# Kernel tuning notes

Measured on AMD Instinct MI355X. Metric: run time of the kernel, lower is better.

## Reference

```python
import jax, jax.numpy as jnp
import numpy as np

D_MODEL = 256
GAMMA = 0.9          # ret_D is built in the torch forward but never applied to the output; kept for fidelity notes
SCALE_BASE = 512     # XPOS default
TEMP = 10000.0
TWO_PI = 2.0 * np.pi


def sine_pos_embed(x):
    """DETR-style 1D sine position embedding with an all-ones mask (as in forward).
    x: [B,T,C] -> pos: [1,T,C] (mask is [1,T] ones, so batch dim broadcasts)."""
    T, C = x.shape[1], x.shape[2]
    x_embed = jnp.arange(1, T + 1, dtype=jnp.float32)          # cumsum of ones
    x_embed = x_embed / (x_embed[-1] + 1e-6) * TWO_PI          # normalize=True
    dim_t = TEMP ** (2.0 * (jnp.arange(C) // 2).astype(jnp.float32) / C)
    pos = x_embed[:, None] / dim_t                             # [T,C]
    pos = jnp.stack([jnp.sin(pos[:, 0::2]), jnp.cos(pos[:, 1::2])], axis=2).reshape(T, C)
    return pos[None].astype(x.dtype)


def _dup_interleave(m):
    # [L, d/2] -> [L, d], columns repeated pairwise: [a,b] -> [a,a,b,b]
    return jnp.repeat(m, 2, axis=-1)


def _rotate_every_two(x):
    x1, x2 = x[..., 0::2], x[..., 1::2]
    return jnp.stack([-x2, x1], axis=-1).reshape(x.shape)


def xpos_apply(x, downscale=False):
    """RetNet XPOS rotary embedding. x: [B,L,d]."""
    L, d = x.shape[1], x.shape[2]
    half = d // 2
    scale_vec = (jnp.arange(0, d, 2, dtype=jnp.float32) + 0.4 * d) / (1.4 * d)   # [d/2]
    power = jnp.arange(L, dtype=jnp.float32) / SCALE_BASE
    scale = scale_vec[None, :] ** power[:, None]                                  # [L, d/2]
    inv_freq = 1.0 / (TEMP ** (jnp.arange(half, dtype=jnp.float32) / half))
    sinusoid = jnp.arange(L, dtype=jnp.float32)[:, None] * inv_freq[None, :]      # [L, d/2]
    sin, cos = jnp.sin(sinusoid), jnp.cos(sinusoid)
    if downscale:
        scale = 1.0 / scale
    sin_s = _dup_interleave(sin * scale)[None].astype(x.dtype)   # [1,L,d]
    cos_s = _dup_interleave(cos * scale)[None].astype(x.dtype)
    return x * cos_s + _rotate_every_two(x) * sin_s


def setup_inputs() -> dict:
    key = jax.random.key(0)
    ks = jax.random.split(key, 8)
    B, TXT, VID, D = 16, 32, 2048, D_MODEL
    S = TXT + VID
    inp = {
        "src": jax.random.normal(ks[0], (B, S, D), dtype=jnp.float32),
        "learn_vid_ret": jax.random.normal(ks[1], (VID * VID, 1), dtype=jnp.float32),
        "W_txt_Q": jax.random.normal(ks[2], (D, D), dtype=jnp.float32) / D,
        "W_txt_K": jax.random.normal(ks[3], (D, D), dtype=jnp.float32) / D,
        "W_txt_V": jax.random.normal(ks[4], (D, D), dtype=jnp.float32) / D,
        "W_vid_Q": jax.random.normal(ks[5], (D, D), dtype=jnp.float32) / D,
        "W_vid_K": jax.random.normal(ks[6], (D, D), dtype=jnp.float32) / D,
        "W_vid_V": jax.random.normal(ks[7], (D, D), dtype=jnp.float32) / D,
        "txt_length": TXT,
    }
    return inp


def reference(src, learn_vid_ret, W_txt_Q, W_txt_K, W_txt_V, W_vid_Q, W_vid_K, W_vid_V, txt_length):
    S = src.shape[1]
    vid_length = S - txt_length

    # learned retention mask over the video block
    learn_ret = jax.nn.sigmoid(learn_vid_ret.reshape(vid_length, vid_length))
    diag = jnp.eye(vid_length, dtype=src.dtype)
    video_ret = (1.0 - diag) * learn_ret
    loss_sparsity = jnp.mean(jnp.abs(video_ret))

    # full [S,S] mask: ones everywhere, sigmoid(learned) on the vid-vid block
    ret_mask = jnp.ones((S, S), dtype=src.dtype).at[txt_length:, txt_length:].set(learn_ret)

    txt_mem = src[:, :txt_length]   # [B,TXT,D]
    vid_mem = src[:, txt_length:]   # [B,VID,D]

    pos = sine_pos_embed(txt_mem)   # [1,TXT,D]
    txt_Q = (pos + txt_mem) @ W_txt_Q
    txt_K = (pos + txt_mem) @ W_txt_K
    vid_Q = xpos_apply(vid_mem @ W_vid_Q)
    vid_K = xpos_apply(vid_mem @ W_vid_K, downscale=True)

    Q = jnp.concatenate([txt_Q, vid_Q], axis=1)                  # [B,S,D]
    K = jnp.concatenate([txt_K, vid_K], axis=1)                  # [B,S,D]
    V = jnp.concatenate([txt_mem @ W_txt_V, vid_mem @ W_vid_V], axis=1)

    # retention: QK^T elementwise-masked (no softmax), then weighted V sum
    scores = jnp.einsum('bsd,btd->bst', Q, K) * ret_mask[None]   # [B,S,S]
    out = scores @ V                                             # [B,S,D]
    return out, loss_sparsity
```

## Files before the change

kernel.cpp:

```cpp
#include <hip/hip_runtime.h>

#define B_   16
#define TXT  32
#define VID  2048
#define D_   256
#define S_   2080
#define SP   2176
#define NKT  34
#define GTOT 17424

typedef unsigned short ushort_t;
typedef __attribute__((ext_vector_type(8))) short short8;
typedef __attribute__((ext_vector_type(4))) short short4v;
typedef __attribute__((ext_vector_type(4))) float f32x4;
typedef __attribute__((ext_vector_type(16))) float f32x16;

__device__ __forceinline__ ushort_t f2bf(float f) {
  unsigned u = __builtin_bit_cast(unsigned, f);
  unsigned r = (u + 0x7FFFu + ((u >> 16) & 1u)) >> 16;
  return (ushort_t)r;
}
__device__ __forceinline__ float bf2f(ushort_t h) {
  unsigned u = ((unsigned)h) << 16;
  return __builtin_bit_cast(float, u);
}

__device__ __forceinline__ void g2l16(void* lds, const void* g) {
  __builtin_amdgcn_global_load_lds(
      (const __attribute__((address_space(1))) char*)g,
      (__attribute__((address_space(3))) char*)lds, 16, 0, 0);
}

__device__ __forceinline__ f32x4 mfma16(short8 a, short8 b, f32x4 c) {
  return __builtin_amdgcn_mfma_f32_16x16x32_bf16(a, b, c, 0, 0, 0);
}
__device__ __forceinline__ f32x16 mfma32(short8 a, short8 b, f32x16 c) {
  return __builtin_amdgcn_mfma_f32_32x32x16_bf16(a, b, c, 0, 0, 0);
}


__global__ void tbl_kernel(float* __restrict__ tbl) {
  int idx = blockIdx.x * 256 + threadIdx.x;
  int n = idx >> 7, i = idx & 127;
  float invf = powf(10000.0f, -(float)i / 128.0f);
  float ang = (float)n * invf;
  float s, co;
  sincosf(ang, &s, &co);
  float sv = ((float)(2 * i) + 102.4f) / 358.4f;
  float sc = powf(sv, (float)n / 512.0f);
  float4 r;
  r.x = co * sc; r.y = s * sc; r.z = co / sc; r.w = s / sc;
  *(float4*)(tbl + (size_t)idx * 4) = r;
}

__global__ void sig_loss_kernel(const float* __restrict__ learn, ushort_t* __restrict__ sigp,
                                float* __restrict__ loss) {
  const int tid = threadIdx.x;
  const int base = (blockIdx.x * 256 + tid) * 8;
  float4 v0 = *(const float4*)(learn + base);
  float4 v1 = *(const float4*)(learn + base + 4);
  float vals[8] = {v0.x, v0.y, v0.z, v0.w, v1.x, v1.y, v1.z, v1.w};
  float acc = 0.f;
  short8 sh;
  #pragma unroll
  for (int j = 0; j < 8; ++j) {
    int idx = base + j;
    float s = 1.0f / (1.0f + expf(-vals[j]));
    sh[j] = (short)f2bf(s);
    int rr = idx >> 11, cc = idx & 2047;
    if (rr != cc) acc += s;
  }
  *(short8*)(sigp + base) = sh;
  __shared__ float red[256];
  red[tid] = acc;
  __syncthreads();
  #pragma unroll
  for (int st = 128; st > 0; st >>= 1) {
    if (tid < st) red[tid] += red[tid + st];
    __syncthreads();
  }
  if (tid == 0) atomicAdd(loss, red[0] * (1.0f / 4194304.0f));
}

__global__ void pad0_kernel(ushort_t* __restrict__ Qp, ushort_t* __restrict__ Ks,
                            ushort_t* __restrict__ VTs) {
  int i = blockIdx.x * 256 + threadIdx.x;
  short8 z = {0, 0, 0, 0, 0, 0, 0, 0};
  if (i < 49152) {
    int bb = i / 3072, rem = i - bb * 3072;
    int row = 2080 + (rem >> 5), c8 = (rem & 31) * 8;
    *(short8*)(Qp + ((size_t)bb * SP + row) * D_ + c8) = z;
  } else if (i < 65536) {
    int j = i - 49152; int bb = j >> 10; int rem = j & 1023;
    int kstep = rem >> 6, ch = rem & 63;
    size_t base = ((size_t)(bb * NKT + 32)) << 14;
    *(short8*)(Ks + base + kstep * 1024 + 512 + ch * 8) = z;
  } else if (i < 81920) {
    int j = i - 65536; int bb = j >> 10; int rem = j & 1023;
    size_t base = (((size_t)(bb * NKT + 32)) << 14) + 8192;
    *(short8*)(VTs + base + rem * 8) = z;
  }
}

__global__ void wt_kernel(const float* __restrict__ Wq, const float* __restrict__ Wk,
                          const float* __restrict__ Wv, ushort_t* __restrict__ WT) {
  __shared__ float t[64][68];
  const int k0 = blockIdx.x * 64, n0 = blockIdx.y * 64, mt = blockIdx.z;
  const float* W = (mt == 0) ? Wq : (mt == 1) ? Wk : Wv;
  int tid = threadIdx.x;
  int r = tid >> 4, cq = (tid & 15) * 4;
  #pragma unroll
  for (int m = 0; m < 4; ++m) {
    int k = m * 16 + r;
    float4 v = *(const float4*)(W + (size_t)(k0 + k) * 256 + n0 + cq);
    t[k][cq] = v.x; t[k][cq + 1] = v.y; t[k][cq + 2] = v.z; t[k][cq + 3] = v.w;
  }
  __syncthreads();
  #pragma unroll
  for (int m = 0; m < 4; ++m) {
    int n = m * 16 + r;
    short4v h;
    h[0] = (short)f2bf(t[cq + 0][n]);
    h[1] = (short)f2bf(t[cq + 1][n]);
    h[2] = (short)f2bf(t[cq + 2][n]);
    h[3] = (short)f2bf(t[cq + 3][n]);
    *(short4v*)(WT + ((size_t)mt * D_ + n0 + n) * D_ + k0 + cq) = h;
  }
}

__global__ void txt_kernel(const float* __restrict__ src,
                           const float* __restrict__ Wq, const float* __restrict__ Wk,
                           const float* __restrict__ Wv,
                           ushort_t* __restrict__ Qp, ushort_t* __restrict__ Ks,
                           ushort_t* __restrict__ VTs) {
  __shared__ float a_s[8][256];
  __shared__ float x_s[8][256];
  const int tg = blockIdx.x;
  const int b  = blockIdx.y;
  const int c  = threadIdx.x;
  #pragma unroll
  for (int t = 0; t < 8; ++t) {
    int row = tg * 8 + t;
    float x = src[((size_t)b * S_ + row) * D_ + c];
    float xe = (float)(row + 1) * (6.283185307179586f / (32.0f + 1e-6f));
    int i = c >> 1;
    float dimt = powf(10000.0f, (2.0f * (float)i) / 256.0f);
    float ang = xe / dimt;
    float pv = (c & 1) ? cosf(ang) : sinf(ang);
    x_s[t][c] = x;
    a_s[t][c] = x + pv;
  }
  __syncthreads();
  float q[8] = {0,0,0,0,0,0,0,0}, k[8] = {0,0,0,0,0,0,0,0}, v[8] = {0,0,0,0,0,0,0,0};
  for (int kk = 0; kk < 256; ++kk) {
    float wq = Wq[(size_t)kk * 256 + c];
    float wk = Wk[(size_t)kk * 256 + c];
    float wv = Wv[(size_t)kk * 256 + c];
    #pragma unroll
    for (int t = 0; t < 8; ++t) {
      q[t] = fmaf(a_s[t][kk], wq, q[t]);
      k[t] = fmaf(a_s[t][kk], wk, k[t]);
      v[t] = fmaf(x_s[t][kk], wv, v[t]);
    }
  }
  #pragma unroll
  for (int t = 0; t < 8; ++t) {
    int row = tg * 8 + t;
    Qp[((size_t)b * SP + row) * D_ + c] = f2bf(q[t]);
    size_t kidx = ((((size_t)(b * NKT)) << 14) + (c >> 4) * 1024 + row * 16 + (c & 15)) ^ (((row >> 2) & 1) << 3);
    Ks[kidx] = f2bf(k[t]);
    size_t vidx = ((((size_t)(b * NKT)) << 14) + (row >> 4) * 4096 + c * 16 + (row & 15)) ^ (((c >> 2) & 1) << 3);
    VTs[vidx] = f2bf(v[t]);
  }
}

__global__ __launch_bounds__(256, 2) void vid_gemm(
    const float* __restrict__ src, const ushort_t* __restrict__ WT,
    const float* __restrict__ tbl,
    ushort_t* __restrict__ Qp, ushort_t* __restrict__ Ks, ushort_t* __restrict__ VTs) {
  __shared__ __align__(16) ushort_t ldsA[64 * 64];
  __shared__ __align__(16) ushort_t ldsB[64 * 64];

  const int rt = blockIdx.x;
  const int b  = blockIdx.y;
  const int ct = blockIdx.z;
  const int nt = ct >> 2;
  const int n0 = (ct & 3) * 64;
  const int tid = threadIdx.x;
  const int wv = tid >> 6, lane = tid & 63, l15 = lane & 15, l4 = lane >> 4;

  f32x4 acc[4];
  #pragma unroll
  for (int t2 = 0; t2 < 4; ++t2) { acc[t2][0] = 0.f; acc[t2][1] = 0.f; acc[t2][2] = 0.f; acc[t2][3] = 0.f; }

  for (int kk = 0; kk < 256; kk += 64) {
    #pragma unroll
    for (int m = 0; m < 4; ++m) {
      int q = m * 256 + tid;
      int r = q >> 4;
      int kc = (q & 15) * 4;
      const float4 v = *(const float4*)(src + ((size_t)b * S_ + TXT + rt * 64 + r) * D_ + kk + kc);
      short4v h;
      h[0] = (short)f2bf(v.x); h[1] = (short)f2bf(v.y);
      h[2] = (short)f2bf(v.z); h[3] = (short)f2bf(v.w);
      int off = ((r << 7) + (kc << 1)) ^ ((r & 7) << 4);
      *(short4v*)((char*)ldsA + off) = h;
    }
    #pragma unroll
    for (int m = 0; m < 2; ++m) {
      int p = (m * 256 + tid) * 16;
      int nl = p >> 7;
      int c = (p & 127) ^ ((nl & 7) << 4);
      g2l16((char*)ldsB + p, (const char*)(WT + ((size_t)nt * D_ + n0 + nl) * D_ + kk) + c);
    }
    __syncthreads();
    #pragma unroll
    for (int ks = 0; ks < 2; ++ks) {
      int ar = wv * 16 + l15;
      int aoff = ((ar << 7) + ((ks * 32 + l4 * 8) << 1)) ^ ((ar & 7) << 4);
      short8 av = *(const short8*)((const char*)ldsA + aoff);
      #pragma unroll
      for (int t2 = 0; t2 < 4; ++t2) {
        int nl = t2 * 16 + l15;
        int boff = ((nl << 7) + ((ks * 32 + l4 * 8) << 1)) ^ ((nl & 7) << 4);
        short8 bv = *(const short8*)((const char*)ldsB + boff);
        acc[t2] = mfma16(av, bv, acc[t2]);
      }
    }
    __syncthreads();
  }

  const int rowl = wv * 16 + l4 * 4;
  if (nt < 2) {
    #pragma unroll
    for (int t2 = 0; t2 < 4; ++t2) {
      int c = n0 + t2 * 16 + l15;
      #pragma unroll
      for (int r = 0; r < 4; ++r) {
        int n = rt * 64 + rowl + r;
        float x = acc[t2][r];
        float xp = __shfl_xor(x, 1);
        const float4 tb = *(const float4*)(tbl + ((size_t)n * 128 + (c >> 1)) * 4);
        float cs = (nt == 0) ? tb.x : tb.z;
        float ss = (nt == 0) ? tb.y : tb.w;
        float val = (c & 1) ? fmaf(x, cs, xp * ss) : fmaf(x, cs, -xp * ss);
        if (nt == 0) {
          Qp[((size_t)b * SP + TXT + n) * D_ + c] = f2bf(val);
        } else {
          int kvg = TXT + n;
          size_t kidx = ((((size_t)(b * NKT + (kvg >> 6))) << 14) + (c >> 4) * 1024 + (kvg & 63) * 16 + (c & 15))
                        ^ (((kvg >> 2) & 1) << 3);
          Ks[kidx] = f2bf(val);
        }
      }
    }
  } else {
    #pragma unroll
    for (int t2 = 0; t2 < 4; ++t2)
      #pragma unroll
      for (int r = 0; r < 4; ++r) {
        int rr = rowl + r;
        int cc = t2 * 16 + l15;
        int off = ((rr << 7) + (cc << 1)) ^ ((rr & 7) << 4);
        *(ushort_t*)((char*)ldsA + off) = f2bf(acc[t2][r]);
      }
    __syncthreads();
    int n = tid >> 2;
    int rc = (tid & 3) * 16;
    short8 o0, o1;
    #pragma unroll
    for (int j = 0; j < 8; ++j) {
      int rr = rc + j;
      int off = ((rr << 7) + (n << 1)) ^ ((rr & 7) << 4);
      o0[j] = *(const short*)((const char*)ldsA + off);
    }
    #pragma unroll
    for (int j = 0; j < 8; ++j) {
      int rr = rc + 8 + j;
      int off = ((rr << 7) + (n << 1)) ^ ((rr & 7) << 4);
      o1[j] = *(const short*)((const char*)ldsA + off);
    }
    int d = n0 + n;
    int kvg0 = TXT + rt * 64 + rc;
    size_t base = (((size_t)(b * NKT + (kvg0 >> 6))) << 14) + ((kvg0 >> 4) & 3) * 4096 + d * 16;
    int swz8 = ((d >> 2) & 1) << 3;
    *(short8*)(VTs + base + swz8) = o0;
    *(short8*)(VTs + base + (swz8 ^ 8)) = o1;
  }
}

__global__ __launch_bounds__(512, 1) void attn_kernel(
    const ushort_t* __restrict__ Qp, const ushort_t* __restrict__ Ks,
    const ushort_t* __restrict__ VTs, const ushort_t* __restrict__ sigp,
    float* __restrict__ out) {
  __shared__ __align__(16) ushort_t Kb[2][16384];
  __shared__ __align__(16) ushort_t Vb[2][16384];
  __shared__ __align__(16) ushort_t Pb[2][4096];

  const int kblk = blockIdx.x;
  const int bs = (kblk & 7) * 32 + (kblk >> 3);
  const int gs = bs * 68 + (bs < 16 ? bs : 16);
  const int ge = gs + 68 + (bs < 16 ? 1 : 0);

  const int tid = threadIdx.x;
  const int wid = tid >> 6, lane = tid & 63;
  const int l31 = lane & 31, l5 = lane >> 5;
  const bool isQK = wid < 4;
  const int qh = (wid >> 1) & 1, kh = wid & 1;
  const int d0 = (wid & 3) * 64;

  int cb_b = gs / 1089;
  int rrem = gs - cb_b * 1089;
  int cb_q = rrem / 33;
  int cb_k = rrem - cb_q * 33;

  auto stage = [&](ushort_t* dst, const ushort_t* srcb, int bb, int tt) {
    const char* src = (const char*)srcb + (((size_t)(bb * NKT + tt)) << 15);
    #pragma unroll
    for (int m = 0; m < 4; ++m) { int s = m * 512 + tid; g2l16((char*)dst + s * 16, src + s * 16); }
  };

  short8 qf[16];
  int4 mq[4];
  const int qloc = qh * 32 + l31;

  auto ldq = [&](int bb, int qq) {
    const ushort_t* qrow = Qp + ((size_t)bb * SP + qq * 64 + qloc) * D_ + l5 * 8;
    #pragma unroll
    for (int ks = 0; ks < 16; ++ks) qf[ks] = *(const short8*)(qrow + ks * 16);
  };
  auto ldmask = [&](int qq, int tt) {
    int q = qq * 64 + qloc;
    int qc = q - TXT; qc = qc < 0 ? 0 : (qc > 2047 ? 2047 : qc);
    int kvp = tt * 64 + kh * 32 - TXT;
    int kvc = (kvp >= 0 && kvp <= 2016) ? kvp : 0;
    const int4* mrow = (const int4*)(sigp + (size_t)qc * 2048 + kvc);
    mq[0] = mrow[0]; mq[1] = mrow[1]; mq[2] = mrow[2]; mq[3] = mrow[3];
  };

  f32x16 oacc[2][2];
  #pragma unroll
  for (int i2 = 0; i2 < 2; ++i2)
    #pragma unroll
    for (int j2 = 0; j2 < 2; ++j2)
      #pragma unroll
      for (int r = 0; r < 16; ++r) oacc[i2][j2][r] = 0.f;

  const int kswz = ((l31 >> 2) & 1) << 4;
  const int pswz = (l31 & 7) << 4;

  int n1_b = cb_b, n1_q = cb_q, n1_k = cb_k;
  if (gs <= ge - 2) { ++n1_k; if (n1_k == 33) { n1_k = 0; ++n1_q; if (n1_q == 33) { n1_q = 0; ++n1_b; } } }
  stage(Kb[gs & 1], Ks, cb_b, cb_k);
  if (isQK) ldmask(cb_q, cb_k);
  stage(Kb[(gs + 1) & 1], Ks, n1_b, n1_k);
  stage(Vb[gs & 1], VTs, cb_b, cb_k);
  if (isQK) { asm volatile("s_waitcnt vmcnt(12)" ::: "memory"); }
  else      { asm volatile("s_waitcnt vmcnt(8)"  ::: "memory"); }
  __builtin_amdgcn_sched_barrier(0);
  __builtin_amdgcn_s_barrier();
  __builtin_amdgcn_sched_barrier(0);

  int pv_b = cb_b, pv_q = cb_q, pv_k = cb_k;

  for (int i = gs; i <= ge; ++i) {
    const int cb = i & 1;
    n1_b = cb_b; n1_q = cb_q; n1_k = cb_k;
    if (i <= ge - 2) { ++n1_k; if (n1_k == 33) { n1_k = 0; ++n1_q; if (n1_q == 33) { n1_q = 0; ++n1_b; } } }
    int n2_b = n1_b, n2_q = n1_q, n2_k = n1_k;
    if (i <= ge - 3) { ++n2_k; if (n2_k == 33) { n2_k = 0; ++n2_q; if (n2_q == 33) { n2_q = 0; ++n2_b; } } }

    if (isQK) {
      if (i < ge) {
        if (cb_k == 0 || i == gs) ldq(cb_b, cb_q);
        f32x16 s0, s1;
        #pragma unroll
        for (int r = 0; r < 16; ++r) { s0[r] = 0.f; s1[r] = 0.f; }
        const int krow = (kh * 32 + l31) * 32 + l5 * 16;
        __builtin_amdgcn_s_setprio(1);
        #pragma unroll
        for (int ks = 0; ks < 8; ++ks) {
          short8 ka = *(const short8*)((const char*)Kb[cb] + ((ks * 2048 + krow) ^ kswz));
          short8 kc = *(const short8*)((const char*)Kb[cb] + (((ks + 8) * 2048 + krow) ^ kswz));
          s0 = mfma32(ka, qf[ks], s0);
          s1 = mfma32(kc, qf[ks + 8], s1);
        }
        __builtin_amdgcn_s_setprio(0);
        {
          int q = cb_q * 64 + qloc;
          bool qv = (q >= TXT) && (q < S_);
          int kvp = cb_k * 64 + kh * 32 - TXT;
          bool kvv = (kvp >= 0 && kvp <= 2016);
          bool ok = qv && kvv;
          const unsigned* mw = (const unsigned*)mq;
          #pragma unroll
          for (int t = 0; t < 4; ++t) {
            unsigned w0p, w1p;
            {
              unsigned wa = mw[4 * t + 0], wb = mw[4 * t + 2];
              unsigned w = l5 ? wb : wa;
              float m0 = ok ? bf2f((ushort_t)(w & 0xFFFFu)) : 1.0f;
              float m1 = ok ? bf2f((ushort_t)(w >> 16)) : 1.0f;
              int r = 4 * t;
              float p0 = (s0[r] + s1[r]) * m0;
              float p1 = (s0[r + 1] + s1[r + 1]) * m1;
              asm("v_cvt_pk_bf16_f32 %0, %1, %2" : "=v"(w0p) : "v"(p0), "v"(p1));
            }
            {
              unsigned wa = mw[4 * t + 1], wb = mw[4 * t + 3];
              unsigned w = l5 ? wb : wa;
              float m0 = ok ? bf2f((ushort_t)(w & 0xFFFFu)) : 1.0f;
              float m1 = ok ? bf2f((ushort_t)(w >> 16)) : 1.0f;
              int r = 4 * t + 2;
              float p0 = (s0[r] + s1[r]) * m0;
              float p1 = (s0[r + 1] + s1[r + 1]) * m1;
              asm("v_cvt_pk_bf16_f32 %0, %1, %2" : "=v"(w1p) : "v"(p0), "v"(p1));
            }
            int off = ((qloc << 7) + (kh << 6) + (t << 4) + (l5 << 3)) ^ pswz;
            *(uint2*)((char*)Pb[cb] + off) = make_uint2(w0p, w1p);
          }
        }
        asm volatile("s_waitcnt lgkmcnt(0)" ::: "memory");
        __builtin_amdgcn_sched_barrier(0);
      }
    } else {
      if (i > gs) {
        const int pbuf = cb ^ 1;
        __builtin_amdgcn_s_setprio(1);
        #pragma unroll
        for (int ks = 0; ks < 4; ++ks) {
          short8 pf0 = *(const short8*)((const char*)Pb[pbuf] + ((l31 * 128 + ks * 32 + l5 * 16) ^ pswz));
          short8 pf1 = *(const short8*)((const char*)Pb[pbuf] + (((32 + l31) * 128 + ks * 32 + l5 * 16) ^ pswz));
          short8 vf0 = *(const short8*)((const char*)Vb[pbuf] + ((ks * 8192 + (d0 + l31) * 32 + l5 * 16) ^ kswz));
          short8 vf1 = *(const short8*)((const char*)Vb[pbuf] + ((ks * 8192 + (d0 + 32 + l31) * 32 + l5 * 16) ^ kswz));
          oacc[0][0] = mfma32(pf0, vf0, oacc[0][0]);
          oacc[0][1] = mfma32(pf0, vf1, oacc[0][1]);
          oacc[1][0] = mfma32(pf1, vf0, oacc[1][0]);
          oacc[1][1] = mfma32(pf1, vf1, oacc[1][1]);
        }
        __builtin_amdgcn_s_setprio(0);
        if (pv_k == 32 || i == ge) {
          #pragma unroll
          for (int qg2 = 0; qg2 < 2; ++qg2)
            #pragma unroll
            for (int dg = 0; dg < 2; ++dg)
              #pragma unroll
              for (int r = 0; r < 16; ++r) {
                int qg = pv_q * 64 + qg2 * 32 + (r & 3) + 8 * (r >> 2) + 4 * l5;
                int dd = d0 + dg * 32 + l31;
                if (qg < S_)
                  unsafeAtomicAdd(&out[((size_t)pv_b * S_ + qg) * D_ + dd], oacc[qg2][dg][r]);
                oacc[qg2][dg][r] = 0.f;
              }
        }
      }
    }

    __builtin_amdgcn_sched_barrier(0);
    __builtin_amdgcn_s_barrier();
    __builtin_amdgcn_sched_barrier(0);

    if (i < ge) {
      if (isQK) ldmask(n1_q, n1_k);
      stage(Kb[cb], Ks, n2_b, n2_k);
      stage(Vb[cb ^ 1], VTs, n1_b, n1_k);
      __builtin_amdgcn_sched_barrier(0);
      if (isQK) { asm volatile("s_waitcnt vmcnt(12)" ::: "memory"); }
      else      { asm volatile("s_waitcnt vmcnt(8)"  ::: "memory"); }
      __builtin_amdgcn_sched_barrier(0);
    }
    __builtin_amdgcn_s_barrier();
    __builtin_amdgcn_sched_barrier(0);

    pv_b = cb_b; pv_q = cb_q; pv_k = cb_k;
    cb_b = n1_b; cb_q = n1_q; cb_k = n1_k;
  }
}

extern "C" void kernel_launch(void* const* d_in, const int* in_sizes, int n_in,
                              void* d_out, int out_size, void* d_ws, size_t ws_size,
                              hipStream_t stream) {
  (void)in_sizes; (void)n_in; (void)ws_size;
  const float* src   = (const float*)d_in[0];
  const float* learn = (const float*)d_in[1];
  const float* Wtq = (const float*)d_in[2];
  const float* Wtk = (const float*)d_in[3];
  const float* Wtv = (const float*)d_in[4];
  const float* Wvq = (const float*)d_in[5];
  const float* Wvk = (const float*)d_in[6];
  const float* Wvv = (const float*)d_in[7];
  float* out = (float*)d_out;

  char* ws = (char*)d_ws;
  const size_t QKV_ONE = (size_t)B_ * SP * D_ * 2;
  const size_t QP_OFF  = 0;
  const size_t KS_OFF  = QP_OFF + QKV_ONE;
  const size_t VT_OFF  = KS_OFF + QKV_ONE;
  const size_t SIG_OFF = VT_OFF + QKV_ONE;
  const size_t TBL_OFF = SIG_OFF + (size_t)VID * VID * 2;
  const size_t WT_OFF  = TBL_OFF + (size_t)VID * 128 * 4 * sizeof(float);

  ushort_t* Qp   = (ushort_t*)(ws + QP_OFF);
  ushort_t* Ks   = (ushort_t*)(ws + KS_OFF);
  ushort_t* VTs  = (ushort_t*)(ws + VT_OFF);
  ushort_t* sigp = (ushort_t*)(ws + SIG_OFF);
  float*    tbl  = (float*)(ws + TBL_OFF);
  ushort_t* WT   = (ushort_t*)(ws + WT_OFF);

  hipMemsetAsync(d_out, 0, (size_t)out_size * sizeof(float), stream);
  pad0_kernel<<<320, 256, 0, stream>>>(Qp, Ks, VTs);
  tbl_kernel<<<1024, 256, 0, stream>>>(tbl);
  sig_loss_kernel<<<2048, 256, 0, stream>>>(learn, sigp, out + (size_t)B_ * S_ * D_);
  wt_kernel<<<dim3(4, 4, 3), 256, 0, stream>>>(Wvq, Wvk, Wvv, WT);
  txt_kernel<<<dim3(4, B_), 256, 0, stream>>>(src, Wtq, Wtk, Wtv, Qp, Ks, VTs);
  vid_gemm<<<dim3(32, B_, 12), 256, 0, stream>>>(src, WT, tbl, Qp, Ks, VTs);
  attn_kernel<<<dim3(256), 512, 0, stream>>>(Qp, Ks, VTs, sigp, out);
}
```

Baseline: 325.6 us.

## Single-buffer attention LDS for higher occupancy and pre-convert video src to bf16

The attention kernel drops double-buffered K/V shared tiles for single buffers, raises the launch-bounds occupancy hint and doubles the grid to 512 blocks, each handling half the tile range. This trades software prefetch depth for more resident blocks to hide latency. Separately, a new cvt_kernel converts the video part of src to bf16 once, so vid_gemm can stream A tiles with direct global-to-LDS copies instead of converting fp32 in each of the 12 column-tile blocks. That costs an extra kernel launch and extra workspace, and it falls back to the old path if the workspace is too small.

```diff
diff --git a/kernel.cpp b/kernel.cpp
--- a/kernel.cpp
+++ b/kernel.cpp
@@ -80,6 +80,20 @@
     __syncthreads();
   }
   if (tid == 0) atomicAdd(loss, red[0] * (1.0f / 4194304.0f));
+}
+
+__global__ void cvt_kernel(const float* __restrict__ src, ushort_t* __restrict__ srcb) {
+  int i = blockIdx.x * 256 + threadIdx.x;
+  int b = i >> 16;
+  int rem = i & 65535;
+  int row = rem >> 5, c8 = (rem & 31) * 8;
+  const float* p = src + ((size_t)b * S_ + TXT + row) * D_ + c8;
+  float4 v0 = *(const float4*)p;
+  float4 v1 = *(const float4*)(p + 4);
+  short8 h;
+  h[0] = (short)f2bf(v0.x); h[1] = (short)f2bf(v0.y); h[2] = (short)f2bf(v0.z); h[3] = (short)f2bf(v0.w);
+  h[4] = (short)f2bf(v1.x); h[5] = (short)f2bf(v1.y); h[6] = (short)f2bf(v1.z); h[7] = (short)f2bf(v1.w);
+  *(short8*)(srcb + ((size_t)b * VID + row) * D_ + c8) = h;
 }
 
 __global__ void pad0_kernel(ushort_t* __restrict__ Qp, ushort_t* __restrict__ Ks,
@@ -174,9 +188,10 @@
   }
 }
 
+template <int MODE>
 __global__ __launch_bounds__(256, 2) void vid_gemm(
-    const float* __restrict__ src, const ushort_t* __restrict__ WT,
-    const float* __restrict__ tbl,
+    const float* __restrict__ src, const ushort_t* __restrict__ srcb,
+    const ushort_t* __restrict__ WT, const float* __restrict__ tbl,
     ushort_t* __restrict__ Qp, ushort_t* __restrict__ Ks, ushort_t* __restrict__ VTs) {
   __shared__ __align__(16) ushort_t ldsA[64 * 64];
   __shared__ __align__(16) ushort_t ldsB[64 * 64];
@@ -194,17 +209,28 @@
   for (int t2 = 0; t2 < 4; ++t2) { acc[t2][0] = 0.f; acc[t2][1] = 0.f; acc[t2][2] = 0.f; acc[t2][3] = 0.f; }
 
   for (int kk = 0; kk < 256; kk += 64) {
-    #pragma unroll
-    for (int m = 0; m < 4; ++m) {
-      int q = m * 256 + tid;
-      int r = q >> 4;
-      int kc = (q & 15) * 4;
-      const float4 v = *(const float4*)(src + ((size_t)b * S_ + TXT + rt * 64 + r) * D_ + kk + kc);
-      short4v h;
-      h[0] = (short)f2bf(v.x); h[1] = (short)f2bf(v.y);
-      h[2] = (short)f2bf(v.z); h[3] = (short)f2bf(v.w);
-      int off = ((r << 7) + (kc << 1)) ^ ((r & 7) << 4);
-      *(short4v*)((char*)ldsA + off) = h;
+    if (MODE == 1) {
+      #pragma unroll
+      for (int m = 0; m < 2; ++m) {
+        int p = (m * 256 + tid) * 16;
+        int r = p >> 7;
+        int cb = (p & 127) ^ ((r & 7) << 4);
+        g2l16((char*)ldsA + p,
+              (const char*)(srcb + ((size_t)b * VID + rt * 64 + r) * D_ + kk) + cb);
+      }
+    } else {
+      #pragma unroll
+      for (int m = 0; m < 4; ++m) {
+        int q = m * 256 + tid;
+        int r = q >> 4;
+        int kc = (q & 15) * 4;
+        const float4 v = *(const float4*)(src + ((size_t)b * S_ + TXT + rt * 64 + r) * D_ + kk + kc);
+        short4v h;
+        h[0] = (short)f2bf(v.x); h[1] = (short)f2bf(v.y);
+        h[2] = (short)f2bf(v.z); h[3] = (short)f2bf(v.w);
+        int off = ((r << 7) + (kc << 1)) ^ ((r & 7) << 4);
+        *(short4v*)((char*)ldsA + off) = h;
+      }
     }
     #pragma unroll
     for (int m = 0; m < 2; ++m) {
@@ -289,18 +315,18 @@
   }
 }
 
-__global__ __launch_bounds__(512, 1) void attn_kernel(
+__global__ __launch_bounds__(512, 4) void attn_kernel(
     const ushort_t* __restrict__ Qp, const ushort_t* __restrict__ Ks,
     const ushort_t* __restrict__ VTs, const ushort_t* __restrict__ sigp,
     float* __restrict__ out) {
-  __shared__ __align__(16) ushort_t Kb[2][16384];
-  __shared__ __align__(16) ushort_t Vb[2][16384];
+  __shared__ __align__(16) ushort_t Kb[16384];
+  __shared__ __align__(16) ushort_t Vb[16384];
   __shared__ __align__(16) ushort_t Pb[2][4096];
 
   const int kblk = blockIdx.x;
-  const int bs = (kblk & 7) * 32 + (kblk >> 3);
-  const int gs = bs * 68 + (bs < 16 ? bs : 16);
-  const int ge = gs + 68 + (bs < 16 ? 1 : 0);
+  const int bs = (kblk & 7) * 64 + (kblk >> 3);
+  const int gs = bs * 34 + (bs >> 5);
+  const int ge = (bs + 1) * 34 + ((bs + 1) >> 5);
 
   const int tid = threadIdx.x;
   const int wid = tid >> 6, lane = tid & 63;
@@ -308,6 +334,7 @@
   const bool isQK = wid < 4;
   const int qh = (wid >> 1) & 1, kh = wid & 1;
   const int d0 = (wid & 3) * 64;
+  const int qloc = qh * 32 + l31;
 
   int cb_b = gs / 1089;
   int rrem = gs - cb_b * 1089;
@@ -322,7 +349,6 @@
 
   short8 qf[16];
   int4 mq[4];
-  const int qloc = qh * 32 + l31;
 
   auto ldq = [&](int bb, int qq) {
     const ushort_t* qrow = Qp + ((size_t)bb * SP + qq * 64 + qloc) * D_ + l5 * 8;
@@ -349,14 +375,9 @@
   const int kswz = ((l31 >> 2) & 1) << 4;
   const int pswz = (l31 & 7) << 4;
 
-  int n1_b = cb_b, n1_q = cb_q, n1_k = cb_k;
-  if (gs <= ge - 2) { ++n1_k; if (n1_k == 33) { n1_k = 0; ++n1_q; if (n1_q == 33) { n1_q = 0; ++n1_b; } } }
-  stage(Kb[gs & 1], Ks, cb_b, cb_k);
   if (isQK) ldmask(cb_q, cb_k);
-  stage(Kb[(gs + 1) & 1], Ks, n1_b, n1_k);
-  stage(Vb[gs & 1], VTs, cb_b, cb_k);
-  if (isQK) { asm volatile("s_waitcnt vmcnt(12)" ::: "memory"); }
-  else      { asm volatile("s_waitcnt vmcnt(8)"  ::: "memory"); }
+  stage(Kb, Ks, cb_b, cb_k);
+  asm volatile("s_waitcnt vmcnt(0)" ::: "memory");
   __builtin_amdgcn_sched_barrier(0);
   __builtin_amdgcn_s_barrier();
   __builtin_amdgcn_sched_barrier(0);
@@ -364,11 +385,8 @@
   int pv_b = cb_b, pv_q = cb_q, pv_k = cb_k;
 
   for (int i = gs; i <= ge; ++i) {
-    const int cb = i & 1;
-    n1_b = cb_b; n1_q = cb_q; n1_k = cb_k;
+    int n1_b = cb_b, n1_q = cb_q, n1_k = cb_k;
     if (i <= ge - 2) { ++n1_k; if (n1_k == 33) { n1_k = 0; ++n1_q; if (n1_q == 33) { n1_q = 0; ++n1_b; } } }
-    int n2_b = n1_b, n2_q = n1_q, n2_k = n1_k;
-    if (i <= ge - 3) { ++n2_k; if (n2_k == 33) { n2_k = 0; ++n2_q; if (n2_q == 33) { n2_q = 0; ++n2_b; } } }
 
     if (isQK) {
       if (i < ge) {
@@ -380,8 +398,8 @@
         __builtin_amdgcn_s_setprio(1);
         #pragma unroll
         for (int ks = 0; ks < 8; ++ks) {
-          short8 ka = *(const short8*)((const char*)Kb[cb] + ((ks * 2048 + krow) ^ kswz));
-          short8 kc = *(const short8*)((const char*)Kb[cb] + (((ks + 8) * 2048 + krow) ^ kswz));
+          short8 ka = *(const short8*)((const char*)Kb + ((ks * 2048 + krow) ^ kswz));
+          short8 kc = *(const short8*)((const char*)Kb + (((ks + 8) * 2048 + krow) ^ kswz));
           s0 = mfma32(ka, qf[ks], s0);
           s1 = mfma32(kc, qf[ks + 8], s1);
         }
@@ -417,7 +435,7 @@
               asm("v_cvt_pk_bf16_f32 %0, %1, %2" : "=v"(w1p) : "v"(p0), "v"(p1));
             }
             int off = ((qloc << 7) + (kh << 6) + (t << 4) + (l5 << 3)) ^ pswz;
-            *(uint2*)((char*)Pb[cb] + off) = make_uint2(w0p, w1p);
+            *(uint2*)((char*)Pb[i & 1] + off) = make_uint2(w0p, w1p);
           }
         }
         asm volatile("s_waitcnt lgkmcnt(0)" ::: "memory");
@@ -425,20 +443,22 @@
       }
     } else {
       if (i > gs) {
-        const int pbuf = cb ^ 1;
+        const int pbuf = (i & 1) ^ 1;
         __builtin_amdgcn_s_setprio(1);
         #pragma unroll
         for (int ks = 0; ks < 4; ++ks) {
           short8 pf0 = *(const short8*)((const char*)Pb[pbuf] + ((l31 * 128 + ks * 32 + l5 * 16) ^ pswz));
           short8 pf1 = *(const short8*)((const char*)Pb[pbuf] + (((32 + l31) * 128 + ks * 32 + l5 * 16) ^ pswz));
-          short8 vf0 = *(const short8*)((const char*)Vb[pbuf] + ((ks * 8192 + (d0 + l31) * 32 + l5 * 16) ^ kswz));
-          short8 vf1 = *(const short8*)((const char*)Vb[pbuf] + ((ks * 8192 + (d0 + 32 + l31) * 32 + l5 * 16) ^ kswz));
+          short8 vf0 = *(const short8*)((const char*)Vb + ((ks * 8192 + (d0 + l31) * 32 + l5 * 16) ^ kswz));
+          short8 vf1 = *(const short8*)((const char*)Vb + ((ks * 8192 + (d0 + 32 + l31) * 32 + l5 * 16) ^ kswz));
           oacc[0][0] = mfma32(pf0, vf0, oacc[0][0]);
           oacc[0][1] = mfma32(pf0, vf1, oacc[0][1]);
           oacc[1][0] = mfma32(pf1, vf0, oacc[1][0]);
           oacc[1][1] = mfma32(pf1, vf1, oacc[1][1]);
         }
         __builtin_amdgcn_s_setprio(0);
+        asm volatile("s_waitcnt lgkmcnt(0)" ::: "memory");
+        __builtin_amdgcn_sched_barrier(0);
         if (pv_k == 32 || i == ge) {
           #pragma unroll
           for (int qg2 = 0; qg2 < 2; ++qg2)
@@ -462,11 +482,11 @@
 
     if (i < ge) {
       if (isQK) ldmask(n1_q, n1_k);
-      stage(Kb[cb], Ks, n2_b, n2_k);
-      stage(Vb[cb ^ 1], VTs, n1_b, n1_k);
+      stage(Kb, Ks, n1_b, n1_k);
+      stage(Vb, VTs, cb_b, cb_k);
       __builtin_amdgcn_sched_barrier(0);
-      if (isQK) { asm volatile("s_waitcnt vmcnt(12)" ::: "memory"); }
-      else      { asm volatile("s_waitcnt vmcnt(8)"  ::: "memory"); }
+      if (isQK) { asm volatile("s_waitcnt vmcnt(4)" ::: "memory"); }
+      else      { asm volatile("s_waitcnt vmcnt(0)" ::: "memory"); }
       __builtin_amdgcn_sched_barrier(0);
     }
     __builtin_amdgcn_s_barrier();
@@ -480,7 +500,7 @@
 extern "C" void kernel_launch(void* const* d_in, const int* in_sizes, int n_in,
                               void* d_out, int out_size, void* d_ws, size_t ws_size,
                               hipStream_t stream) {
-  (void)in_sizes; (void)n_in; (void)ws_size;
+  (void)in_sizes; (void)n_in;
   const float* src   = (const float*)d_in[0];
   const float* learn = (const float*)d_in[1];
   const float* Wtq = (const float*)d_in[2];
@@ -492,13 +512,15 @@
   float* out = (float*)d_out;
 
   char* ws = (char*)d_ws;
-  const size_t QKV_ONE = (size_t)B_ * SP * D_ * 2;
-  const size_t QP_OFF  = 0;
-  const size_t KS_OFF  = QP_OFF + QKV_ONE;
-  const size_t VT_OFF  = KS_OFF + QKV_ONE;
-  const size_t SIG_OFF = VT_OFF + QKV_ONE;
-  const size_t TBL_OFF = SIG_OFF + (size_t)VID * VID * 2;
-  const size_t WT_OFF  = TBL_OFF + (size_t)VID * 128 * 4 * sizeof(float);
+  const size_t QKV_ONE  = (size_t)B_ * SP * D_ * 2;
+  const size_t QP_OFF   = 0;
+  const size_t KS_OFF   = QP_OFF + QKV_ONE;
+  const size_t VT_OFF   = KS_OFF + QKV_ONE;
+  const size_t SIG_OFF  = VT_OFF + QKV_ONE;
+  const size_t TBL_OFF  = SIG_OFF + (size_t)VID * VID * 2;
+  const size_t WT_OFF   = TBL_OFF + (size_t)VID * 128 * 4 * sizeof(float);
+  const size_t SRCB_OFF = WT_OFF + (size_t)3 * D_ * D_ * 2;
+  const size_t NEED_SRCB = SRCB_OFF + (size_t)B_ * VID * D_ * 2;
 
   ushort_t* Qp   = (ushort_t*)(ws + QP_OFF);
   ushort_t* Ks   = (ushort_t*)(ws + KS_OFF);
@@ -506,6 +528,7 @@
   ushort_t* sigp = (ushort_t*)(ws + SIG_OFF);
   float*    tbl  = (float*)(ws + TBL_OFF);
   ushort_t* WT   = (ushort_t*)(ws + WT_OFF);
+  ushort_t* srcb = (ushort_t*)(ws + SRCB_OFF);
 
   hipMemsetAsync(d_out, 0, (size_t)out_size * sizeof(float), stream);
   pad0_kernel<<<320, 256, 0, stream>>>(Qp, Ks, VTs);
@@ -513,6 +536,11 @@
   sig_loss_kernel<<<2048, 256, 0, stream>>>(learn, sigp, out + (size_t)B_ * S_ * D_);
   wt_kernel<<<dim3(4, 4, 3), 256, 0, stream>>>(Wvq, Wvk, Wvv, WT);
   txt_kernel<<<dim3(4, B_), 256, 0, stream>>>(src, Wtq, Wtk, Wtv, Qp, Ks, VTs);
-  vid_gemm<<<dim3(32, B_, 12), 256, 0, stream>>>(src, WT, tbl, Qp, Ks, VTs);
-  attn_kernel<<<dim3(256), 512, 0, stream>>>(Qp, Ks, VTs, sigp, out);
-}
+  if (ws_size >= NEED_SRCB) {
+    cvt_kernel<<<4096, 256, 0, stream>>>(src, srcb);
+    vid_gemm<1><<<dim3(32, B_, 12), 256, 0, stream>>>(src, srcb, WT, tbl, Qp, Ks, VTs);
+  } else {
+    vid_gemm<0><<<dim3(32, B_, 12), 256, 0, stream>>>(src, srcb, WT, tbl, Qp, Ks, VTs);
+  }
+  attn_kernel<<<dim3(512), 512, 0, stream>>>(Qp, Ks, VTs, sigp, out);
+}
```

Result: slower. 640.2 us (+96.6%).
